# Kernel tuning notes

Hardware: AMD Instinct MI355X
Metric: run time of the kernel (lower is better)

Reference implementation:

```python
import jax, jax.numpy as jnp
import numpy as np

H = 8       # heads
DH = 64     # dim_head
EPS = 1e-5  # LayerNorm eps (torch default)


def _ln(x, g, b):
    m = x.mean(-1, keepdims=True)
    v = x.var(-1, keepdims=True)
    return (x - m) / jnp.sqrt(v + EPS) * g + b


def setup_inputs() -> dict:
    key = jax.random.key(0)
    ks = jax.random.split(key, 8)
    B, N, D = 2, 2048, 512
    s = lambda k, shape: jax.random.normal(k, shape, jnp.float32) * 0.02
    return {
        "q": jax.random.normal(ks[0], (B, N, D), jnp.float32),
        "k": jax.random.normal(ks[1], (B, N, D), jnp.float32),
        "v": jax.random.normal(ks[2], (B, N, D), jnp.float32),
        "ln_g": jnp.ones((D,), jnp.float32),
        "ln_b": jnp.zeros((D,), jnp.float32),
        "W_in": s(ks[3], (H * DH, D)),          # Linear(dim, inner_dim, bias=False)
        "wp_w1": s(ks[4], (DH, 2 * DH)),         # Linear(2*dim_head, dim_head)
        "wp_b1": jnp.zeros((DH,), jnp.float32),
        "wp_ln_g": jnp.ones((DH,), jnp.float32),
        "wp_ln_b": jnp.zeros((DH,), jnp.float32),
        "wp_w2": s(ks[5], (1, DH)),              # Linear(dim_head, 1)
        "wp_b2": jnp.zeros((1,), jnp.float32),
        "W_out": s(ks[6], (D, H * DH)),          # Linear(inner_dim, dim)
        "b_out": jnp.zeros((D,), jnp.float32),
    }


def reference(q, k, v, ln_g, ln_b, W_in, wp_w1, wp_b1, wp_ln_g, wp_ln_b,
              wp_w2, wp_b2, W_out, b_out):
    B, N, D = q.shape

    def proj(t):
        x = _ln(t, ln_g, ln_b) @ W_in.T                 # [B, N, H*DH]
        return x.reshape(B, N, H, DH).transpose(2, 0, 1, 3)  # [H, B, N, DH]

    fq, fk, fv = proj(q), proj(k), proj(v)

    # cosine similarity component
    dots = jnp.einsum('hbnd,hbmd->hbnm', fq, fk)        # [H, B, N, N]
    qn = jnp.linalg.norm(fq, axis=-1)                   # [H, B, N]
    kn = jnp.linalg.norm(fk, axis=-1)
    cosine = dots / (qn[..., :, None] * kn[..., None, :])

    # mean-centered covariance component
    qc = fq - fq.mean(-1, keepdims=True)
    kc = fk - fk.mean(-1, keepdims=True)
    cov = jnp.einsum('hbnd,hbmd->hbnm', qc, kc) / DH    # [H, B, N, N]

    # dynamic per-head blend weight
    qg = fq.mean((1, 2))                                # [H, DH]
    kg = fk.mean((1, 2))
    feat = jnp.concatenate([qg, kg], axis=-1)           # [H, 2*DH]
    hid = jax.nn.relu(_ln(feat @ wp_w1.T + wp_b1, wp_ln_g, wp_ln_b))
    w = jax.nn.sigmoid(hid @ wp_w2.T + wp_b2)           # [H, 1]
    w = w.reshape(H, 1, 1, 1)

    blend = (1.0 - w) * cosine + w * cov                # no softmax in cosine variant
    out = jnp.einsum('hbnm,hbmd->hbnd', blend, fv)      # [H, B, N, DH]
    out = out.transpose(1, 2, 0, 3).reshape(B, N, H * DH)
    return out @ W_out.T + b_out
```

## Files before the change

### kernel.cpp

```cpp
#include <hip/hip_runtime.h>
#include <stdint.h>

#define CH 8
#define CDH 64
#define CB 2
#define CN 2048
#define CD 512

typedef float f32x4 __attribute__((ext_vector_type(4)));
typedef __bf16 bf16x8 __attribute__((ext_vector_type(8)));
typedef unsigned short u16;
typedef unsigned int u32;

#define MFMA(a, b, c) __builtin_amdgcn_mfma_f32_16x16x32_bf16((a), (b), (c), 0, 0, 0)
#define GLOAD16(g, l)                                                              \
  __builtin_amdgcn_global_load_lds((const __attribute__((address_space(1))) void*)(g), \
                                   (__attribute__((address_space(3))) void*)(l), 16, 0, 0)

__device__ __forceinline__ u16 f2bf(float f) {
  union { float f; unsigned u; } c; c.f = f;
  return (u16)((c.u + 0x7FFFu + ((c.u >> 16) & 1u)) >> 16);
}
__device__ __forceinline__ float bf2f(u16 h) {
  union { unsigned u; float f; } c; c.u = ((unsigned)h) << 16;
  return c.f;
}

__global__ __launch_bounds__(256) void ln_convw_kernel(const float* __restrict__ q,
                                                       const float* __restrict__ k,
                                                       const float* __restrict__ v,
                                                       const float* __restrict__ g,
                                                       const float* __restrict__ bb,
                                                       u16* __restrict__ xln,
                                                       const float* __restrict__ wi_f,
                                                       const float* __restrict__ wo_f,
                                                       u16* __restrict__ wi,
                                                       u16* __restrict__ wo) {
  int row = blockIdx.x;
  int tid = threadIdx.x;
  if (row >= 12288) {
    int i = (row - 12288) * 256 + tid;
    wi[i] = f2bf(wi_f[i]);
    wo[i] = f2bf(wo_f[i]);
    return;
  }
  int t = row >> 12;
  int rr = row & 4095;
  const float* src = (t == 0 ? q : (t == 1 ? k : v)) + (size_t)rr * CD;
  float x0 = src[tid], x1 = src[tid + 256];
  float s = x0 + x1, s2 = x0 * x0 + x1 * x1;
#pragma unroll
  for (int m = 1; m < 64; m <<= 1) { s += __shfl_xor(s, m); s2 += __shfl_xor(s2, m); }
  __shared__ float red[8];
  int w = tid >> 6;
  if ((tid & 63) == 0) { red[w] = s; red[4 + w] = s2; }
  __syncthreads();
  s = red[0] + red[1] + red[2] + red[3];
  s2 = red[4] + red[5] + red[6] + red[7];
  float mean = s * (1.f / 512.f);
  float var = s2 * (1.f / 512.f) - mean * mean;
  float rstd = rsqrtf(var + 1e-5f);
  u16* dst = xln + (size_t)row * CD;
  dst[tid]       = f2bf((x0 - mean) * rstd * g[tid] + bb[tid]);
  dst[tid + 256] = f2bf((x1 - mean) * rstd * g[tid + 256] + bb[tid + 256]);
}

template <int OUT_BF16, int ADD_BIAS, int MODE>
__global__ __launch_bounds__(256) void gemm_bt(const u16* __restrict__ A,
                                               const u16* __restrict__ Bt,
                                               void* __restrict__ Cout,
                                               const float* __restrict__ bias,
                                               float* __restrict__ iqn,
                                               float* __restrict__ ikn,
                                               float* __restrict__ qgp,
                                               float* __restrict__ kgp,
                                               u16* __restrict__ fkT,
                                               u16* __restrict__ fvT) {
  __shared__ u16 S[4][8192];
#define AL_(s) (S[s])
#define BL_(s) (S[2 + (s)])
  int tm = blockIdx.x * 128, tn = blockIdx.y * 128;
  int tid = threadIdx.x;
  int w = tid >> 6, l = tid & 63;
  int wr = w >> 1, wc = w & 1;
  int lo = l & 15, hi = l >> 4;

  f32x4 zz = {0.f, 0.f, 0.f, 0.f};
  f32x4 acc[4][4];
#pragma unroll
  for (int mi = 0; mi < 4; mi++)
#pragma unroll
    for (int ni = 0; ni < 4; ni++) acc[mi][ni] = zz;

  int rowA = 8 * w + (l >> 3);
  int sl = l & 7;

#pragma unroll
  for (int i = 0; i < 4; i++) {
    int rl = rowA + 32 * i;
    int sp = sl ^ (rl & 7);
    GLOAD16(A + (size_t)(tm + rl) * CD + sp * 8, (char*)AL_(0) + w * 1024 + i * 4096);
    GLOAD16(Bt + (size_t)(tn + rl) * CD + sp * 8, (char*)BL_(0) + w * 1024 + i * 4096);
  }
  __syncthreads();

  int cur = 0;
  for (int kt = 0; kt < 8; ++kt) {
    if (kt + 1 < 8) {
      int nxt = cur ^ 1;
#pragma unroll
      for (int i = 0; i < 4; i++) {
        int rl = rowA + 32 * i;
        int sp = sl ^ (rl & 7);
        GLOAD16(A + (size_t)(tm + rl) * CD + (kt + 1) * 64 + sp * 8,
                (char*)AL_(nxt) + w * 1024 + i * 4096);
        GLOAD16(Bt + (size_t)(tn + rl) * CD + (kt + 1) * 64 + sp * 8,
                (char*)BL_(nxt) + w * 1024 + i * 4096);
      }
    }
    const u16* Ac = AL_(cur);
    const u16* Bc = BL_(cur);
#pragma unroll
    for (int kk = 0; kk < 2; kk++) {
      bf16x8 af[4], bfr[4];
#pragma unroll
      for (int mi = 0; mi < 4; mi++) {
        int row = wr * 64 + mi * 16 + lo;
        int slot = (hi + 4 * kk) ^ (row & 7);
        af[mi] = *(const bf16x8*)&Ac[row * 64 + slot * 8];
      }
#pragma unroll
      for (int ni = 0; ni < 4; ni++) {
        int row = wc * 64 + ni * 16 + lo;
        int slot = (hi + 4 * kk) ^ (row & 7);
        bfr[ni] = *(const bf16x8*)&Bc[row * 64 + slot * 8];
      }
#pragma unroll
      for (int mi = 0; mi < 4; mi++)
#pragma unroll
        for (int ni = 0; ni < 4; ni++)
          acc[mi][ni] = MFMA(af[mi], bfr[ni], acc[mi][ni]);
    }
    if (kt + 1 < 8) {
      __syncthreads();
      cur ^= 1;
    }
  }

  if (MODE == 1) {
    int tblk = blockIdx.x;
    int h = blockIdx.y * 2 + wc;
    if (tblk < 32) {
#pragma unroll
      for (int mi = 0; mi < 4; mi++)
#pragma unroll
        for (int rg = 0; rg < 4; rg++) {
          float s2 = 0.f;
#pragma unroll
          for (int ni = 0; ni < 4; ni++) {
            float vv = acc[mi][ni][rg];
            s2 += vv * vv;
          }
#pragma unroll
          for (int m = 1; m < 16; m <<= 1) s2 += __shfl_xor(s2, m);
          if (lo == 0) {
            int rloc = tm + wr * 64 + mi * 16 + hi * 4 + rg;
            int b = rloc >> 11, n = rloc & 2047;
            iqn[((size_t)h * 2 + b) * CN + n] = rsqrtf(s2);
          }
        }
      float cs[4];
#pragma unroll
      for (int ni = 0; ni < 4; ni++) {
        float s = 0.f;
#pragma unroll
        for (int mi = 0; mi < 4; mi++)
#pragma unroll
          for (int rg = 0; rg < 4; rg++) s += acc[mi][ni][rg];
        s += __shfl_xor(s, 16);
        s += __shfl_xor(s, 32);
        cs[ni] = s;
      }
      __syncthreads();
      float* redl = (float*)&S[0][0];
      if (hi == 0)
#pragma unroll
        for (int ni = 0; ni < 4; ni++) redl[((wr * 2 + wc) * 4 + ni) * 16 + lo] = cs[ni];
      __syncthreads();
      if (wr == 0 && hi == 0) {
#pragma unroll
        for (int ni = 0; ni < 4; ni++) {
          float vsum = redl[((0 * 2 + wc) * 4 + ni) * 16 + lo] +
                       redl[((1 * 2 + wc) * 4 + ni) * 16 + lo];
          qgp[(tblk * 8 + h) * 64 + ni * 16 + lo] = vsum;
        }
      }
    } else {
      bool isk = tblk < 64;
      u16* dstT = isk ? fkT : fvT;
      int rloc0 = tm - (isk ? 4096 : 8192);
      int bb2 = rloc0 >> 11, n0 = rloc0 & 2047;
      float csk[4];
      if (isk) {
#pragma unroll
        for (int mi = 0; mi < 4; mi++)
#pragma unroll
          for (int rg = 0; rg < 4; rg++) {
            float s2 = 0.f;
#pragma unroll
            for (int ni = 0; ni < 4; ni++) {
              float vv = acc[mi][ni][rg];
              s2 += vv * vv;
            }
#pragma unroll
            for (int m = 1; m < 16; m <<= 1) s2 += __shfl_xor(s2, m);
            if (lo == 0) {
              int n = n0 + wr * 64 + mi * 16 + hi * 4 + rg;
              ikn[((size_t)h * 2 + bb2) * CN + n] = rsqrtf(s2);
            }
          }
#pragma unroll
        for (int ni = 0; ni < 4; ni++) {
          float s = 0.f;
#pragma unroll
          for (int mi = 0; mi < 4; mi++)
#pragma unroll
            for (int rg = 0; rg < 4; rg++) s += acc[mi][ni][rg];
          s += __shfl_xor(s, 16);
          s += __shfl_xor(s, 32);
          csk[ni] = s;
        }
      }
      __syncthreads();
      u16* Sf = &S[0][0];
      int reg = wc * 2 + wr;
#pragma unroll
      for (int mi = 0; mi < 4; mi++)
#pragma unroll
        for (int ni = 0; ni < 4; ni++) {
          int d = ni * 16 + lo;
          int m0 = mi * 16 + hi * 4;
          u16 t4[4];
#pragma unroll
          for (int rg = 0; rg < 4; rg++) t4[rg] = f2bf(acc[mi][ni][rg]);
          int off = (reg * 64 + d) * 64 + (m0 ^ ((d & 7) << 3));
          *(uint2*)&Sf[off] = *(const uint2*)t4;
        }
      __syncthreads();
      {
        int head = tid >> 7, c = tid & 127;
        int hg = blockIdx.y * 2 + head;
        size_t base = ((size_t)(hg * 2 + bb2)) * 64 * CN;
#pragma unroll
        for (int p = 0; p < 8; p++) {
          int flat = p * 128 + c;
          int d = flat >> 4, mc = flat & 15;
          int wr2 = mc >> 3, m64 = (mc & 7) * 8;
          int off = ((head * 2 + wr2) * 64 + d) * 64 + (m64 ^ ((d & 7) << 3));
          bf16x8 vv = *(const bf16x8*)&Sf[off];
          *(bf16x8*)&dstT[base + (size_t)d * CN + n0 + mc * 8] = vv;
        }
      }
      if (isk) {
        __syncthreads();
        float* redl = (float*)&S[0][0];
        if (hi == 0)
#pragma unroll
          for (int ni = 0; ni < 4; ni++) redl[((wr * 2 + wc) * 4 + ni) * 16 + lo] = csk[ni];
        __syncthreads();
        if (wr == 0 && hi == 0) {
#pragma unroll
          for (int ni = 0; ni < 4; ni++) {
            float vsum = redl[((0 * 2 + wc) * 4 + ni) * 16 + lo] +
                         redl[((1 * 2 + wc) * 4 + ni) * 16 + lo];
            kgp[((tblk - 32) * 8 + h) * 64 + ni * 16 + lo] = vsum;
          }
        }
      }
      return;
    }
  }

#pragma unroll
  for (int mi = 0; mi < 4; mi++)
#pragma unroll
    for (int ni = 0; ni < 4; ni++) {
      int col = tn + wc * 64 + ni * 16 + lo;
      float bv = ADD_BIAS ? bias[col] : 0.f;
#pragma unroll
      for (int rg = 0; rg < 4; rg++) {
        int rowg = tm + wr * 64 + mi * 16 + hi * 4 + rg;
        float vout = acc[mi][ni][rg] + bv;
        if (OUT_BF16)
          ((u16*)Cout)[(size_t)rowg * CD + col] = f2bf(vout);
        else
          ((float*)Cout)[(size_t)rowg * CD + col] = vout;
      }
    }
#undef AL_
#undef BL_
}

__global__ __launch_bounds__(256) void gemm_M(const u16* __restrict__ fkT,
                                              const u16* __restrict__ fvT,
                                              const float* __restrict__ ikn,
                                              float* __restrict__ Mpart) {
  int bid = blockIdx.x;
  int hb = bid & 15, ms = bid >> 4;
  int tid = threadIdx.x, w = tid >> 6, l = tid & 63;
  int lo = l & 15, hi = l >> 4;

  __shared__ u16 GM[6][4096];
#define AK_(s) (GM[s])
#define AKH_(s) (GM[2 + (s)])
#define BV_(s) (GM[4 + (s)])

  const u16* Ab = fkT + (size_t)hb * 64 * CN;
  const u16* Vb = fvT + (size_t)hb * 64 * CN;
  const float* ikb = ikn + (size_t)hb * CN;

  f32x4 zz = {0.f, 0.f, 0.f, 0.f};
  f32x4 acc[2][4];
#pragma unroll
  for (int mat = 0; mat < 2; mat++)
#pragma unroll
    for (int dt = 0; dt < 4; dt++) acc[mat][dt] = zz;

  int rls = 8 * w + (l >> 3);
  int sls = l & 7;

  bf16x8 areg[2];
  f32x4 ikreg[2][2];

  auto STAGEGL = [&](int kt, int slot) {
    int mc = ms * 512 + kt * 64;
#pragma unroll
    for (int i = 0; i < 2; i++) {
      int row = rls + 32 * i;
      int sp = sls ^ (row & 7);
      GLOAD16(Ab + (size_t)row * CN + mc + sp * 8, (char*)AK_(slot) + w * 1024 + i * 4096);
      GLOAD16(Vb + (size_t)row * CN + mc + sp * 8, (char*)BV_(slot) + w * 1024 + i * 4096);
    }
  };
  auto LOADA = [&](int kt) {
    int mc = ms * 512 + kt * 64;
#pragma unroll
    for (int i = 0; i < 2; i++) {
      int row = rls + 32 * i;
      int sp = sls ^ (row & 7);
      areg[i] = *(const bf16x8*)&Ab[(size_t)row * CN + mc + sp * 8];
      ikreg[i][0] = *(const f32x4*)&ikb[mc + sp * 8];
      ikreg[i][1] = *(const f32x4*)&ikb[mc + sp * 8 + 4];
    }
  };
  auto WRITEA = [&](int slot) {
#pragma unroll
    for (int i = 0; i < 2; i++) {
      u16 outp[8];
#pragma unroll
      for (int j = 0; j < 4; j++) outp[j] = f2bf((float)areg[i][j] * ikreg[i][0][j]);
#pragma unroll
      for (int j = 0; j < 4; j++) outp[4 + j] = f2bf((float)areg[i][4 + j] * ikreg[i][1][j]);
      *(bf16x8*)((char*)AKH_(slot) + w * 1024 + i * 4096 + l * 16) = *(const bf16x8*)outp;
    }
  };

  LOADA(0);
  STAGEGL(0, 0);
  WRITEA(0);
  __syncthreads();

  int cur = 0;
  for (int kt = 0; kt < 8; ++kt) {
    if (kt + 1 < 8) {
      LOADA(kt + 1);
      STAGEGL(kt + 1, cur ^ 1);
    }
#pragma unroll
    for (int kk = 0; kk < 2; kk++) {
      int arow = w * 16 + lo;
      int aslot = (hi + 4 * kk) ^ (arow & 7);
      bf16x8 af = *(const bf16x8*)&AK_(cur)[arow * 64 + aslot * 8];
      bf16x8 afh = *(const bf16x8*)&AKH_(cur)[arow * 64 + aslot * 8];
#pragma unroll
      for (int dt = 0; dt < 4; dt++) {
        int brow = dt * 16 + lo;
        int bslot = (hi + 4 * kk) ^ (brow & 7);
        bf16x8 bv = *(const bf16x8*)&BV_(cur)[brow * 64 + bslot * 8];
        acc[0][dt] = MFMA(afh, bv, acc[0][dt]);
        acc[1][dt] = MFMA(af, bv, acc[1][dt]);
      }
    }
    if (kt + 1 < 8) {
      WRITEA(cur ^ 1);
      __syncthreads();
      cur ^= 1;
    }
  }

  float* outp = Mpart + ((size_t)(hb * 4 + ms)) * 8192;
#pragma unroll
  for (int mat = 0; mat < 2; mat++)
#pragma unroll
    for (int dt = 0; dt < 4; dt++) {
      int d = dt * 16 + lo;
#pragma unroll
      for (int rg = 0; rg < 4; rg++) {
        int j = mat * 64 + w * 16 + hi * 4 + rg;
        outp[j * 64 + d] = acc[mat][dt][rg];
      }
    }
#undef AK_
#undef AKH_
#undef BV_
}

__global__ __launch_bounds__(256) void reduceM_mlp(const float* __restrict__ Mpart,
                                                   const float* __restrict__ qgp,
                                                   const float* __restrict__ kgp,
                                                   const float* __restrict__ w1,
                                                   const float* __restrict__ b1,
                                                   const float* __restrict__ lng,
                                                   const float* __restrict__ lnb,
                                                   const float* __restrict__ w2,
                                                   const float* __restrict__ b2,
                                                   u16* __restrict__ Bmat) {
  int hb = blockIdx.x;
  int h = hb >> 1;
  int tid = threadIdx.x;
  __shared__ float qg[64], kg[64], abg[3];
  if (tid < 64) {
    float s1 = 0.f, s2 = 0.f;
#pragma unroll
    for (int c = 0; c < 32; c++) {
      s1 += qgp[(c * 8 + h) * 64 + tid];
      s2 += kgp[(c * 8 + h) * 64 + tid];
    }
    qg[tid] = s1 * (1.f / 4096.f);
    kg[tid] = s2 * (1.f / 4096.f);
  }
  __syncthreads();
  if (tid < 64) {
    float acc = b1[tid];
#pragma unroll 8
    for (int i = 0; i < 64; i++)
      acc += qg[i] * w1[tid * 128 + i] + kg[i] * w1[tid * 128 + 64 + i];
    float s1 = acc, s2 = acc * acc;
#pragma unroll
    for (int m = 1; m < 64; m <<= 1) { s1 += __shfl_xor(s1, m); s2 += __shfl_xor(s2, m); }
    float mean = s1 * (1.f / 64.f);
    float var = s2 * (1.f / 64.f) - mean * mean;
    float y = (acc - mean) * rsqrtf(var + 1e-5f) * lng[tid] + lnb[tid];
    float hid = fmaxf(y, 0.f);
    float t = hid * w2[tid];
#pragma unroll
    for (int m = 1; m < 64; m <<= 1) t += __shfl_xor(t, m);
    float wv = 1.f / (1.f + expf(-(t + b2[0])));
    if (tid == 0) { abg[0] = 1.f - wv; abg[1] = wv * (1.f / 64.f); abg[2] = wv; }
  }
  __syncthreads();
  float alpha = abg[0], beta = abg[1], gamma = abg[2];

  __shared__ float Ms[128 * 65];
  __shared__ float S2s[64];
#pragma unroll
  for (int e = 0; e < 32; e++) {
    int idx = e * 256 + tid;
    int j = idx >> 6, d = idx & 63;
    float s = 0.f;
#pragma unroll
    for (int ms = 0; ms < 4; ms++)
      s += Mpart[((size_t)(hb * 4 + ms)) * 8192 + idx];
    Ms[j * 65 + d] = s;
  }
  __syncthreads();
  if (tid < 64) {
    float s = 0.f;
#pragma unroll
    for (int i = 0; i < 64; i++) s += Ms[(64 + i) * 65 + tid];
    S2s[tid] = s;
  }
  __syncthreads();
#pragma unroll
  for (int e = 0; e < 32; e++) {
    int idx = e * 256 + tid;
    int jr = idx >> 6, ic = idx & 63;
    float v;
    if (jr < 64) v = alpha * Ms[ic * 65 + jr];
    else {
      int d = jr - 64;
      v = beta * Ms[(64 + ic) * 65 + d] - (gamma * (1.f / 4096.f)) * S2s[d];
    }
    Bmat[(size_t)hb * 8192 + idx] = f2bf(v);
  }
}

__global__ __launch_bounds__(256) void gemm_out(const u16* __restrict__ F0,
                                                const u16* __restrict__ Bmat,
                                                const float* __restrict__ iqn,
                                                u16* __restrict__ A2) {
  int bid = blockIdx.x;
  int hb = bid >> 4, qt = bid & 15;
  int b = hb & 1, h = hb >> 1;
  int tid = threadIdx.x, w = tid >> 6, l = tid & 63;
  int lo = l & 15, hi = l >> 4;
  int qbase = qt * 128;

  const u16* Bm = Bmat + (size_t)hb * 8192;
  bf16x8 bm[8][2];
#pragma unroll
  for (int jt = 0; jt < 8; jt++)
#pragma unroll
    for (int kk = 0; kk < 2; kk++)
      bm[jt][kk] = *(const bf16x8*)&Bm[(jt * 16 + lo) * 64 + hi * 8 + kk * 32];

  f32x4 zz = {0.f, 0.f, 0.f, 0.f};
  f32x4 acc[2][8];
#pragma unroll
  for (int f = 0; f < 2; f++)
#pragma unroll
    for (int jt = 0; jt < 8; jt++) acc[f][jt] = zz;

#pragma unroll
  for (int f = 0; f < 2; f++) {
    const u16* qp = F0 + ((size_t)(b * CN + qbase + w * 32 + f * 16 + lo)) * CD +
                    h * 64 + hi * 8;
    bf16x8 a0 = *(const bf16x8*)qp;
    bf16x8 a1 = *(const bf16x8*)(qp + 32);
#pragma unroll
    for (int jt = 0; jt < 8; jt++) {
      acc[f][jt] = MFMA(a0, bm[jt][0], acc[f][jt]);
      acc[f][jt] = MFMA(a1, bm[jt][1], acc[f][jt]);
    }
  }

  const float* iqn_hb = iqn + (size_t)hb * CN;
#pragma unroll
  for (int f = 0; f < 2; f++) {
    float iqv[4];
    int nb = qbase + w * 32 + f * 16 + hi * 4;
#pragma unroll
    for (int rg = 0; rg < 4; rg++) iqv[rg] = iqn_hb[nb + rg];
#pragma unroll
    for (int jt = 0; jt < 4; jt++) {
      int d = jt * 16 + lo;
#pragma unroll
      for (int rg = 0; rg < 4; rg++) {
        float vout = iqv[rg] * acc[f][jt][rg] + acc[f][jt + 4][rg];
        int n = nb + rg;
        A2[((size_t)(b * CN + n)) * CD + h * 64 + d] = f2bf(vout);
      }
    }
  }
}

extern "C" void kernel_launch(void* const* d_in, const int* in_sizes, int n_in,
                              void* d_out, int out_size, void* d_ws, size_t ws_size,
                              hipStream_t stream) {
  const float* q = (const float*)d_in[0];
  const float* k = (const float*)d_in[1];
  const float* v = (const float*)d_in[2];
  const float* ln_g = (const float*)d_in[3];
  const float* ln_b = (const float*)d_in[4];
  const float* W_in = (const float*)d_in[5];
  const float* wp_w1 = (const float*)d_in[6];
  const float* wp_b1 = (const float*)d_in[7];
  const float* wp_lng = (const float*)d_in[8];
  const float* wp_lnb = (const float*)d_in[9];
  const float* wp_w2 = (const float*)d_in[10];
  const float* wp_b2 = (const float*)d_in[11];
  const float* W_out = (const float*)d_in[12];
  const float* b_out = (const float*)d_in[13];

  char* ws = (char*)d_ws;
  u16* xln = (u16*)(ws + 0);
  u16* F0 = (u16*)(ws + 12582912);
  u16* Wi = (u16*)(ws + 16777216);
  u16* Wo = (u16*)(ws + 17301504);
  u16* fkT = (u16*)(ws + 17825792);
  u16* fvT = (u16*)(ws + 22020096);
  u16* A2 = (u16*)(ws + 26214400);
  float* iqn = (float*)(ws + 30408704);
  float* ikn = (float*)(ws + 30539776);
  float* qgp = (float*)(ws + 30670848);
  float* kgp = (float*)(ws + 30736384);
  float* Mpart = (float*)(ws + 30801920);
  u16* Bmat = (u16*)(ws + 32899072);

  ln_convw_kernel<<<13312, 256, 0, stream>>>(q, k, v, ln_g, ln_b, xln,
                                             W_in, W_out, Wi, Wo);
  gemm_bt<1, 0, 1><<<dim3(96, 4), 256, 0, stream>>>(xln, Wi, (void*)F0, nullptr,
                                                    iqn, ikn, qgp, kgp, fkT, fvT);
  gemm_M<<<64, 256, 0, stream>>>(fkT, fvT, ikn, Mpart);
  reduceM_mlp<<<16, 256, 0, stream>>>(Mpart, qgp, kgp, wp_w1, wp_b1,
                                      wp_lng, wp_lnb, wp_w2, wp_b2, Bmat);
  gemm_out<<<256, 256, 0, stream>>>(F0, Bmat, iqn, A2);
  gemm_bt<0, 1, 0><<<dim3(32, 4), 256, 0, stream>>>(A2, Wo, d_out, b_out,
                                                    nullptr, nullptr, nullptr,
                                                    nullptr, nullptr, nullptr);
}
```

Measured before the change: 61.54 us.

## Fold per-head blend matrices into output projection and merge launches

The per-head KV matrices are folded into the output projection weights, giving a per-batch 1024-wide combined weight. The final GEMM then reads a concatenated [normalized q | raw q] activation, which removes the separate gemm_out pass, the A2 intermediate and the iqn buffer. The M reduction and the blend-weight MLP are merged into one 16-block kernel that runs the full 2048-long reduction without split partials, cutting two launches. The trade-off is a lower-parallelism M kernel (16 blocks instead of 64), a doubled K in the final GEMM, and a larger F0 write.

```diff
diff --git a/kernel.cpp b/kernel.cpp
--- a/kernel.cpp
+++ b/kernel.cpp
@@ -10,7 +10,6 @@
 typedef float f32x4 __attribute__((ext_vector_type(4)));
 typedef __bf16 bf16x8 __attribute__((ext_vector_type(8)));
 typedef unsigned short u16;
-typedef unsigned int u32;
 
 #define MFMA(a, b, c) __builtin_amdgcn_mfma_f32_16x16x32_bf16((a), (b), (c), 0, 0, 0)
 #define GLOAD16(g, l)                                                              \
@@ -65,17 +64,14 @@
   dst[tid + 256] = f2bf((x1 - mean) * rstd * g[tid + 256] + bb[tid + 256]);
 }
 
-template <int OUT_BF16, int ADD_BIAS, int MODE>
-__global__ __launch_bounds__(256) void gemm_bt(const u16* __restrict__ A,
-                                               const u16* __restrict__ Bt,
-                                               void* __restrict__ Cout,
-                                               const float* __restrict__ bias,
-                                               float* __restrict__ iqn,
-                                               float* __restrict__ ikn,
-                                               float* __restrict__ qgp,
-                                               float* __restrict__ kgp,
-                                               u16* __restrict__ fkT,
-                                               u16* __restrict__ fvT) {
+__global__ __launch_bounds__(256) void gemm1(const u16* __restrict__ A,
+                                             const u16* __restrict__ Bt,
+                                             u16* __restrict__ F0cat,
+                                             float* __restrict__ ikn,
+                                             float* __restrict__ qgp,
+                                             float* __restrict__ kgp,
+                                             u16* __restrict__ fkT,
+                                             u16* __restrict__ fvT) {
   __shared__ u16 S[4][8192];
 #define AL_(s) (S[s])
 #define BL_(s) (S[2 + (s)])
@@ -147,10 +143,70 @@
     }
   }
 
-  if (MODE == 1) {
-    int tblk = blockIdx.x;
-    int h = blockIdx.y * 2 + wc;
-    if (tblk < 32) {
+  int tblk = blockIdx.x;
+  int h = blockIdx.y * 2 + wc;
+  if (tblk < 32) {
+    float rsq[4][4];
+#pragma unroll
+    for (int mi = 0; mi < 4; mi++)
+#pragma unroll
+      for (int rg = 0; rg < 4; rg++) {
+        float s2 = 0.f;
+#pragma unroll
+        for (int ni = 0; ni < 4; ni++) {
+          float vv = acc[mi][ni][rg];
+          s2 += vv * vv;
+        }
+#pragma unroll
+        for (int m = 1; m < 16; m <<= 1) s2 += __shfl_xor(s2, m);
+        rsq[mi][rg] = rsqrtf(s2);
+      }
+    float cs[4];
+#pragma unroll
+    for (int ni = 0; ni < 4; ni++) {
+      float s = 0.f;
+#pragma unroll
+      for (int mi = 0; mi < 4; mi++)
+#pragma unroll
+        for (int rg = 0; rg < 4; rg++) s += acc[mi][ni][rg];
+      s += __shfl_xor(s, 16);
+      s += __shfl_xor(s, 32);
+      cs[ni] = s;
+    }
+    __syncthreads();
+    float* redl = (float*)&S[0][0];
+    if (hi == 0)
+#pragma unroll
+      for (int ni = 0; ni < 4; ni++) redl[((wr * 2 + wc) * 4 + ni) * 16 + lo] = cs[ni];
+    __syncthreads();
+    if (wr == 0 && hi == 0) {
+#pragma unroll
+      for (int ni = 0; ni < 4; ni++) {
+        float vsum = redl[((0 * 2 + wc) * 4 + ni) * 16 + lo] +
+                     redl[((1 * 2 + wc) * 4 + ni) * 16 + lo];
+        qgp[(tblk * 8 + h) * 64 + ni * 16 + lo] = vsum;
+      }
+    }
+#pragma unroll
+    for (int mi = 0; mi < 4; mi++)
+#pragma unroll
+      for (int ni = 0; ni < 4; ni++) {
+        int gcol = tn + wc * 64 + ni * 16 + lo;
+#pragma unroll
+        for (int rg = 0; rg < 4; rg++) {
+          int rowg = tm + wr * 64 + mi * 16 + hi * 4 + rg;
+          float vv = acc[mi][ni][rg];
+          F0cat[(size_t)rowg * 1024 + gcol] = f2bf(rsq[mi][rg] * vv);
+          F0cat[(size_t)rowg * 1024 + 512 + gcol] = f2bf(vv);
+        }
+      }
+  } else {
+    bool isk = tblk < 64;
+    u16* dstT = isk ? fkT : fvT;
+    int rloc0 = tm - (isk ? 4096 : 8192);
+    int bb2 = rloc0 >> 11, n0 = rloc0 & 2047;
+    float csk[4];
+    if (isk) {
 #pragma unroll
       for (int mi = 0; mi < 4; mi++)
 #pragma unroll
@@ -164,12 +220,10 @@
 #pragma unroll
           for (int m = 1; m < 16; m <<= 1) s2 += __shfl_xor(s2, m);
           if (lo == 0) {
-            int rloc = tm + wr * 64 + mi * 16 + hi * 4 + rg;
-            int b = rloc >> 11, n = rloc & 2047;
-            iqn[((size_t)h * 2 + b) * CN + n] = rsqrtf(s2);
+            int n = n0 + wr * 64 + mi * 16 + hi * 4 + rg;
+            ikn[((size_t)h * 2 + bb2) * CN + n] = rsqrtf(s2);
           }
         }
-      float cs[4];
 #pragma unroll
       for (int ni = 0; ni < 4; ni++) {
         float s = 0.f;
@@ -179,134 +233,70 @@
           for (int rg = 0; rg < 4; rg++) s += acc[mi][ni][rg];
         s += __shfl_xor(s, 16);
         s += __shfl_xor(s, 32);
-        cs[ni] = s;
-      }
+        csk[ni] = s;
+      }
+    }
+    __syncthreads();
+    u16* Sf = &S[0][0];
+    int reg = wc * 2 + wr;
+#pragma unroll
+    for (int mi = 0; mi < 4; mi++)
+#pragma unroll
+      for (int ni = 0; ni < 4; ni++) {
+        int d = ni * 16 + lo;
+        int m0 = mi * 16 + hi * 4;
+        u16 t4[4];
+#pragma unroll
+        for (int rg = 0; rg < 4; rg++) t4[rg] = f2bf(acc[mi][ni][rg]);
+        int off = (reg * 64 + d) * 64 + (m0 ^ ((d & 7) << 3));
+        *(uint2*)&Sf[off] = *(const uint2*)t4;
+      }
+    __syncthreads();
+    {
+      int head = tid >> 7, c = tid & 127;
+      int hg = blockIdx.y * 2 + head;
+      size_t base = ((size_t)(hg * 2 + bb2)) * 64 * CN;
+#pragma unroll
+      for (int p = 0; p < 8; p++) {
+        int flat = p * 128 + c;
+        int d = flat >> 4, mc = flat & 15;
+        int wr2 = mc >> 3, m64 = (mc & 7) * 8;
+        int off = ((head * 2 + wr2) * 64 + d) * 64 + (m64 ^ ((d & 7) << 3));
+        bf16x8 vv = *(const bf16x8*)&Sf[off];
+        *(bf16x8*)&dstT[base + (size_t)d * CN + n0 + mc * 8] = vv;
+      }
+    }
+    if (isk) {
       __syncthreads();
       float* redl = (float*)&S[0][0];
       if (hi == 0)
 #pragma unroll
-        for (int ni = 0; ni < 4; ni++) redl[((wr * 2 + wc) * 4 + ni) * 16 + lo] = cs[ni];
+        for (int ni = 0; ni < 4; ni++) redl[((wr * 2 + wc) * 4 + ni) * 16 + lo] = csk[ni];
       __syncthreads();
       if (wr == 0 && hi == 0) {
 #pragma unroll
         for (int ni = 0; ni < 4; ni++) {
           float vsum = redl[((0 * 2 + wc) * 4 + ni) * 16 + lo] +
                        redl[((1 * 2 + wc) * 4 + ni) * 16 + lo];
-          qgp[(tblk * 8 + h) * 64 + ni * 16 + lo] = vsum;
+          kgp[((tblk - 32) * 8 + h) * 64 + ni * 16 + lo] = vsum;
         }
       }
-    } else {
-      bool isk = tblk < 64;
-      u16* dstT = isk ? fkT : fvT;
-      int rloc0 = tm - (isk ? 4096 : 8192);
-      int bb2 = rloc0 >> 11, n0 = rloc0 & 2047;
-      float csk[4];
-      if (isk) {
-#pragma unroll
-        for (int mi = 0; mi < 4; mi++)
-#pragma unroll
-          for (int rg = 0; rg < 4; rg++) {
-            float s2 = 0.f;
-#pragma unroll
-            for (int ni = 0; ni < 4; ni++) {
-              float vv = acc[mi][ni][rg];
-              s2 += vv * vv;
-            }
-#pragma unroll
-            for (int m = 1; m < 16; m <<= 1) s2 += __shfl_xor(s2, m);
-            if (lo == 0) {
-              int n = n0 + wr * 64 + mi * 16 + hi * 4 + rg;
-              ikn[((size_t)h * 2 + bb2) * CN + n] = rsqrtf(s2);
-            }
-          }
-#pragma unroll
-        for (int ni = 0; ni < 4; ni++) {
-          float s = 0.f;
-#pragma unroll
-          for (int mi = 0; mi < 4; mi++)
-#pragma unroll
-            for (int rg = 0; rg < 4; rg++) s += acc[mi][ni][rg];
-          s += __shfl_xor(s, 16);
-          s += __shfl_xor(s, 32);
-          csk[ni] = s;
-        }
-      }
-      __syncthreads();
-      u16* Sf = &S[0][0];
-      int reg = wc * 2 + wr;
-#pragma unroll
-      for (int mi = 0; mi < 4; mi++)
-#pragma unroll
-        for (int ni = 0; ni < 4; ni++) {
-          int d = ni * 16 + lo;
-          int m0 = mi * 16 + hi * 4;
-          u16 t4[4];
-#pragma unroll
-          for (int rg = 0; rg < 4; rg++) t4[rg] = f2bf(acc[mi][ni][rg]);
-          int off = (reg * 64 + d) * 64 + (m0 ^ ((d & 7) << 3));
-          *(uint2*)&Sf[off] = *(const uint2*)t4;
-        }
-      __syncthreads();
-      {
-        int head = tid >> 7, c = tid & 127;
-        int hg = blockIdx.y * 2 + head;
-        size_t base = ((size_t)(hg * 2 + bb2)) * 64 * CN;
-#pragma unroll
-        for (int p = 0; p < 8; p++) {
-          int flat = p * 128 + c;
-          int d = flat >> 4, mc = flat & 15;
-          int wr2 = mc >> 3, m64 = (mc & 7) * 8;
-          int off = ((head * 2 + wr2) * 64 + d) * 64 + (m64 ^ ((d & 7) << 3));
-          bf16x8 vv = *(const bf16x8*)&Sf[off];
-          *(bf16x8*)&dstT[base + (size_t)d * CN + n0 + mc * 8] = vv;
-        }
-      }
-      if (isk) {
-        __syncthreads();
-        float* redl = (float*)&S[0][0];
-        if (hi == 0)
-#pragma unroll
-          for (int ni = 0; ni < 4; ni++) redl[((wr * 2 + wc) * 4 + ni) * 16 + lo] = csk[ni];
-        __syncthreads();
-        if (wr == 0 && hi == 0) {
-#pragma unroll
-          for (int ni = 0; ni < 4; ni++) {
-            float vsum = redl[((0 * 2 + wc) * 4 + ni) * 16 + lo] +
-                         redl[((1 * 2 + wc) * 4 + ni) * 16 + lo];
-            kgp[((tblk - 32) * 8 + h) * 64 + ni * 16 + lo] = vsum;
-          }
-        }
-      }
-      return;
-    }
-  }
-
-#pragma unroll
-  for (int mi = 0; mi < 4; mi++)
-#pragma unroll
-    for (int ni = 0; ni < 4; ni++) {
-      int col = tn + wc * 64 + ni * 16 + lo;
-      float bv = ADD_BIAS ? bias[col] : 0.f;
-#pragma unroll
-      for (int rg = 0; rg < 4; rg++) {
-        int rowg = tm + wr * 64 + mi * 16 + hi * 4 + rg;
-        float vout = acc[mi][ni][rg] + bv;
-        if (OUT_BF16)
-          ((u16*)Cout)[(size_t)rowg * CD + col] = f2bf(vout);
-        else
-          ((float*)Cout)[(size_t)rowg * CD + col] = vout;
-      }
-    }
+    }
+  }
 #undef AL_
 #undef BL_
 }
 
-__global__ __launch_bounds__(256) void gemm_M(const u16* __restrict__ fkT,
-                                              const u16* __restrict__ fvT,
-                                              const float* __restrict__ ikn,
-                                              float* __restrict__ Mpart) {
-  int bid = blockIdx.x;
-  int hb = bid & 15, ms = bid >> 4;
+__global__ __launch_bounds__(256) void gemm_M_mlp_w(
+    const u16* __restrict__ fkT, const u16* __restrict__ fvT,
+    const float* __restrict__ ikn, const float* __restrict__ qgp,
+    const float* __restrict__ kgp, const float* __restrict__ w1,
+    const float* __restrict__ b1, const float* __restrict__ lng,
+    const float* __restrict__ lnb, const float* __restrict__ w2,
+    const float* __restrict__ b2, const u16* __restrict__ Wo,
+    u16* __restrict__ Wbig) {
+  int hb = blockIdx.x;
+  int h = hb >> 1, b = hb & 1;
   int tid = threadIdx.x, w = tid >> 6, l = tid & 63;
   int lo = l & 15, hi = l >> 4;
 
@@ -314,6 +304,38 @@
 #define AK_(s) (GM[s])
 #define AKH_(s) (GM[2 + (s)])
 #define BV_(s) (GM[4 + (s)])
+  __shared__ float abg[3];
+  __shared__ float Msf[64][65];
+  __shared__ float S2s[64];
+  __shared__ u16 M1b[64 * 72];
+  __shared__ u16 Cb[64 * 72];
+
+  if (tid < 64) {
+    float s1 = 0.f, s2 = 0.f;
+#pragma unroll
+    for (int c = 0; c < 32; c++) {
+      s1 += qgp[(c * 8 + h) * 64 + tid];
+      s2 += kgp[(c * 8 + h) * 64 + tid];
+    }
+    Msf[0][tid] = s1 * (1.f / 4096.f);
+    Msf[1][tid] = s2 * (1.f / 4096.f);
+    float acc = b1[tid];
+#pragma unroll 8
+    for (int i = 0; i < 64; i++)
+      acc += Msf[0][i] * w1[tid * 128 + i] + Msf[1][i] * w1[tid * 128 + 64 + i];
+    float t1 = acc, t2 = acc * acc;
+#pragma unroll
+    for (int m = 1; m < 64; m <<= 1) { t1 += __shfl_xor(t1, m); t2 += __shfl_xor(t2, m); }
+    float mean = t1 * (1.f / 64.f);
+    float var = t2 * (1.f / 64.f) - mean * mean;
+    float y = (acc - mean) * rsqrtf(var + 1e-5f) * lng[tid] + lnb[tid];
+    float hid = fmaxf(y, 0.f);
+    float t = hid * w2[tid];
+#pragma unroll
+    for (int m = 1; m < 64; m <<= 1) t += __shfl_xor(t, m);
+    float wv = 1.f / (1.f + expf(-(t + b2[0])));
+    if (tid == 0) { abg[0] = 1.f - wv; abg[1] = wv * (1.f / 64.f); abg[2] = wv; }
+  }
 
   const u16* Ab = fkT + (size_t)hb * 64 * CN;
   const u16* Vb = fvT + (size_t)hb * 64 * CN;
@@ -328,12 +350,11 @@
 
   int rls = 8 * w + (l >> 3);
   int sls = l & 7;
-
   bf16x8 areg[2];
   f32x4 ikreg[2][2];
 
   auto STAGEGL = [&](int kt, int slot) {
-    int mc = ms * 512 + kt * 64;
+    int mc = kt * 64;
 #pragma unroll
     for (int i = 0; i < 2; i++) {
       int row = rls + 32 * i;
@@ -343,7 +364,7 @@
     }
   };
   auto LOADA = [&](int kt) {
-    int mc = ms * 512 + kt * 64;
+    int mc = kt * 64;
 #pragma unroll
     for (int i = 0; i < 2; i++) {
       int row = rls + 32 * i;
@@ -371,8 +392,8 @@
   __syncthreads();
 
   int cur = 0;
-  for (int kt = 0; kt < 8; ++kt) {
-    if (kt + 1 < 8) {
+  for (int kt = 0; kt < 32; ++kt) {
+    if (kt + 1 < 32) {
       LOADA(kt + 1);
       STAGEGL(kt + 1, cur ^ 1);
     }
@@ -391,167 +412,160 @@
         acc[1][dt] = MFMA(af, bv, acc[1][dt]);
       }
     }
-    if (kt + 1 < 8) {
+    if (kt + 1 < 32) {
       WRITEA(cur ^ 1);
       __syncthreads();
       cur ^= 1;
     }
   }
 
-  float* outp = Mpart + ((size_t)(hb * 4 + ms)) * 8192;
-#pragma unroll
-  for (int mat = 0; mat < 2; mat++)
-#pragma unroll
-    for (int dt = 0; dt < 4; dt++) {
-      int d = dt * 16 + lo;
+  __syncthreads();
+#pragma unroll
+  for (int dt = 0; dt < 4; dt++)
+#pragma unroll
+    for (int rg = 0; rg < 4; rg++)
+      Msf[w * 16 + hi * 4 + rg][dt * 16 + lo] = acc[1][dt][rg];
+  __syncthreads();
+  if (tid < 64) {
+    float s = 0.f;
+#pragma unroll
+    for (int i = 0; i < 64; i++) s += Msf[i][tid];
+    S2s[tid] = s;
+  }
+  __syncthreads();
+
+  float alpha = abg[0], beta = abg[1], g4 = abg[2] * (1.f / 4096.f);
+#pragma unroll
+  for (int dt = 0; dt < 4; dt++)
+#pragma unroll
+    for (int rg = 0; rg < 4; rg++) {
+      int i = w * 16 + hi * 4 + rg, d = dt * 16 + lo;
+      M1b[i * 72 + d] = f2bf(alpha * acc[0][dt][rg]);
+      Cb[i * 72 + d] = f2bf(beta * acc[1][dt][rg] - g4 * S2s[d]);
+    }
+  __syncthreads();
+
+  u16* Wb = Wbig + (size_t)b * 512 * 1024;
+#pragma unroll
+  for (int rf = 0; rf < 8; rf++) {
+    int dbase = w * 128 + rf * 16;
+    bf16x8 af[2];
+#pragma unroll
+    for (int kk = 0; kk < 2; kk++)
+      af[kk] = *(const bf16x8*)&Wo[(size_t)(dbase + lo) * 512 + h * 64 + kk * 32 + hi * 8];
+    f32x4 a1[4], a2[4];
+#pragma unroll
+    for (int cf = 0; cf < 4; cf++) { a1[cf] = zz; a2[cf] = zz; }
+#pragma unroll
+    for (int kk = 0; kk < 2; kk++)
+#pragma unroll
+      for (int cf = 0; cf < 4; cf++) {
+        bf16x8 m1 = *(const bf16x8*)&M1b[(cf * 16 + lo) * 72 + kk * 32 + hi * 8];
+        bf16x8 cb = *(const bf16x8*)&Cb[(cf * 16 + lo) * 72 + kk * 32 + hi * 8];
+        a1[cf] = MFMA(af[kk], m1, a1[cf]);
+        a2[cf] = MFMA(af[kk], cb, a2[cf]);
+      }
+#pragma unroll
+    for (int cf = 0; cf < 4; cf++)
 #pragma unroll
       for (int rg = 0; rg < 4; rg++) {
-        int j = mat * 64 + w * 16 + hi * 4 + rg;
-        outp[j * 64 + d] = acc[mat][dt][rg];
-      }
-    }
+        int dout = dbase + hi * 4 + rg;
+        int icol = cf * 16 + lo;
+        Wb[(size_t)dout * 1024 + h * 64 + icol] = f2bf(a1[cf][rg]);
+        Wb[(size_t)dout * 1024 + 512 + h * 64 + icol] = f2bf(a2[cf][rg]);
+      }
+  }
 #undef AK_
 #undef AKH_
 #undef BV_
 }
 
-__global__ __launch_bounds__(256) void reduceM_mlp(const float* __restrict__ Mpart,
-                                                   const float* __restrict__ qgp,
-                                                   const float* __restrict__ kgp,
-                                                   const float* __restrict__ w1,
-                                                   const float* __restrict__ b1,
-                                                   const float* __restrict__ lng,
-                                                   const float* __restrict__ lnb,
-                                                   const float* __restrict__ w2,
-                                                   const float* __restrict__ b2,
-                                                   u16* __restrict__ Bmat) {
-  int hb = blockIdx.x;
-  int h = hb >> 1;
+__global__ __launch_bounds__(256) void gemm_final(const u16* __restrict__ A,
+                                                  const u16* __restrict__ Wbig,
+                                                  const float* __restrict__ bias,
+                                                  float* __restrict__ Cout) {
+  __shared__ u16 Al[2][128 * 64];
+  __shared__ u16 Bl[2][128 * 64];
+  int tm = blockIdx.x * 128, tn = blockIdx.y * 128;
+  const u16* Bt = Wbig + (size_t)(tm >> 11) * 512 * 1024;
   int tid = threadIdx.x;
-  __shared__ float qg[64], kg[64], abg[3];
-  if (tid < 64) {
-    float s1 = 0.f, s2 = 0.f;
-#pragma unroll
-    for (int c = 0; c < 32; c++) {
-      s1 += qgp[(c * 8 + h) * 64 + tid];
-      s2 += kgp[(c * 8 + h) * 64 + tid];
-    }
-    qg[tid] = s1 * (1.f / 4096.f);
-    kg[tid] = s2 * (1.f / 4096.f);
-  }
-  __syncthreads();
-  if (tid < 64) {
-    float acc = b1[tid];
-#pragma unroll 8
-    for (int i = 0; i < 64; i++)
-      acc += qg[i] * w1[tid * 128 + i] + kg[i] * w1[tid * 128 + 64 + i];
-    float s1 = acc, s2 = acc * acc;
-#pragma unroll
-    for (int m = 1; m < 64; m <<= 1) { s1 += __shfl_xor(s1, m); s2 += __shfl_xor(s2, m); }
-    float mean = s1 * (1.f / 64.f);
-    float var = s2 * (1.f / 64.f) - mean * mean;
-    float y = (acc - mean) * rsqrtf(var + 1e-5f) * lng[tid] + lnb[tid];
-    float hid = fmaxf(y, 0.f);
-    float t = hid * w2[tid];
-#pragma unroll
-    for (int m = 1; m < 64; m <<= 1) t += __shfl_xor(t, m);
-    float wv = 1.f / (1.f + expf(-(t + b2[0])));
-    if (tid == 0) { abg[0] = 1.f - wv; abg[1] = wv * (1.f / 64.f); abg[2] = wv; }
-  }
-  __syncthreads();
-  float alpha = abg[0], beta = abg[1], gamma = abg[2];
-
-  __shared__ float Ms[128 * 65];
-  __shared__ float S2s[64];
-#pragma unroll
-  for (int e = 0; e < 32; e++) {
-    int idx = e * 256 + tid;
-    int j = idx >> 6, d = idx & 63;
-    float s = 0.f;
-#pragma unroll
-    for (int ms = 0; ms < 4; ms++)
-      s += Mpart[((size_t)(hb * 4 + ms)) * 8192 + idx];
-    Ms[j * 65 + d] = s;
-  }
-  __syncthreads();
-  if (tid < 64) {
-    float s = 0.f;
-#pragma unroll
-    for (int i = 0; i < 64; i++) s += Ms[(64 + i) * 65 + tid];
-    S2s[tid] = s;
-  }
-  __syncthreads();
-#pragma unroll
-  for (int e = 0; e < 32; e++) {
-    int idx = e * 256 + tid;
-    int jr = idx >> 6, ic = idx & 63;
-    float v;
-    if (jr < 64) v = alpha * Ms[ic * 65 + jr];
-    else {
-      int d = jr - 64;
-      v = beta * Ms[(64 + ic) * 65 + d] - (gamma * (1.f / 4096.f)) * S2s[d];
-    }
-    Bmat[(size_t)hb * 8192 + idx] = f2bf(v);
-  }
-}
-
-__global__ __launch_bounds__(256) void gemm_out(const u16* __restrict__ F0,
-                                                const u16* __restrict__ Bmat,
-                                                const float* __restrict__ iqn,
-                                                u16* __restrict__ A2) {
-  int bid = blockIdx.x;
-  int hb = bid >> 4, qt = bid & 15;
-  int b = hb & 1, h = hb >> 1;
-  int tid = threadIdx.x, w = tid >> 6, l = tid & 63;
+  int w = tid >> 6, l = tid & 63;
+  int wr = w >> 1, wc = w & 1;
   int lo = l & 15, hi = l >> 4;
-  int qbase = qt * 128;
-
-  const u16* Bm = Bmat + (size_t)hb * 8192;
-  bf16x8 bm[8][2];
-#pragma unroll
-  for (int jt = 0; jt < 8; jt++)
-#pragma unroll
-    for (int kk = 0; kk < 2; kk++)
-      bm[jt][kk] = *(const bf16x8*)&Bm[(jt * 16 + lo) * 64 + hi * 8 + kk * 32];
 
   f32x4 zz = {0.f, 0.f, 0.f, 0.f};
-  f32x4 acc[2][8];
-#pragma unroll
-  for (int f = 0; f < 2; f++)
-#pragma unroll
-    for (int jt = 0; jt < 8; jt++) acc[f][jt] = zz;
-
-#pragma unroll
-  for (int f = 0; f < 2; f++) {
-    const u16* qp = F0 + ((size_t)(b * CN + qbase + w * 32 + f * 16 + lo)) * CD +
-                    h * 64 + hi * 8;
-    bf16x8 a0 = *(const bf16x8*)qp;
-    bf16x8 a1 = *(const bf16x8*)(qp + 32);
-#pragma unroll
-    for (int jt = 0; jt < 8; jt++) {
-      acc[f][jt] = MFMA(a0, bm[jt][0], acc[f][jt]);
-      acc[f][jt] = MFMA(a1, bm[jt][1], acc[f][jt]);
-    }
-  }
-
-  const float* iqn_hb = iqn + (size_t)hb * CN;
-#pragma unroll
-  for (int f = 0; f < 2; f++) {
-    float iqv[4];
-    int nb = qbase + w * 32 + f * 16 + hi * 4;
-#pragma unroll
-    for (int rg = 0; rg < 4; rg++) iqv[rg] = iqn_hb[nb + rg];
-#pragma unroll
-    for (int jt = 0; jt < 4; jt++) {
-      int d = jt * 16 + lo;
+  f32x4 acc[4][4];
+#pragma unroll
+  for (int mi = 0; mi < 4; mi++)
+#pragma unroll
+    for (int ni = 0; ni < 4; ni++) acc[mi][ni] = zz;
+
+  int rowA = 8 * w + (l >> 3);
+  int sl = l & 7;
+
+#pragma unroll
+  for (int i = 0; i < 4; i++) {
+    int rl = rowA + 32 * i;
+    int sp = sl ^ (rl & 7);
+    GLOAD16(A + (size_t)(tm + rl) * 1024 + sp * 8, (char*)Al[0] + w * 1024 + i * 4096);
+    GLOAD16(Bt + (size_t)(tn + rl) * 1024 + sp * 8, (char*)Bl[0] + w * 1024 + i * 4096);
+  }
+  __syncthreads();
+
+  int cur = 0;
+  for (int kt = 0; kt < 16; ++kt) {
+    if (kt + 1 < 16) {
+      int nxt = cur ^ 1;
+#pragma unroll
+      for (int i = 0; i < 4; i++) {
+        int rl = rowA + 32 * i;
+        int sp = sl ^ (rl & 7);
+        GLOAD16(A + (size_t)(tm + rl) * 1024 + (kt + 1) * 64 + sp * 8,
+                (char*)Al[nxt] + w * 1024 + i * 4096);
+        GLOAD16(Bt + (size_t)(tn + rl) * 1024 + (kt + 1) * 64 + sp * 8,
+                (char*)Bl[nxt] + w * 1024 + i * 4096);
+      }
+    }
+    const u16* Ac = Al[cur];
+    const u16* Bc = Bl[cur];
+#pragma unroll
+    for (int kk = 0; kk < 2; kk++) {
+      bf16x8 af[4], bfr[4];
+#pragma unroll
+      for (int mi = 0; mi < 4; mi++) {
+        int row = wr * 64 + mi * 16 + lo;
+        int slot = (hi + 4 * kk) ^ (row & 7);
+        af[mi] = *(const bf16x8*)&Ac[row * 64 + slot * 8];
+      }
+#pragma unroll
+      for (int ni = 0; ni < 4; ni++) {
+        int row = wc * 64 + ni * 16 + lo;
+        int slot = (hi + 4 * kk) ^ (row & 7);
+        bfr[ni] = *(const bf16x8*)&Bc[row * 64 + slot * 8];
+      }
+#pragma unroll
+      for (int mi = 0; mi < 4; mi++)
+#pragma unroll
+        for (int ni = 0; ni < 4; ni++)
+          acc[mi][ni] = MFMA(af[mi], bfr[ni], acc[mi][ni]);
+    }
+    if (kt + 1 < 16) {
+      __syncthreads();
+      cur ^= 1;
+    }
+  }
+#pragma unroll
+  for (int mi = 0; mi < 4; mi++)
+#pragma unroll
+    for (int ni = 0; ni < 4; ni++) {
+      int col = tn + wc * 64 + ni * 16 + lo;
+      float bv = bias[col];
 #pragma unroll
       for (int rg = 0; rg < 4; rg++) {
-        float vout = iqv[rg] * acc[f][jt][rg] + acc[f][jt + 4][rg];
-        int n = nb + rg;
-        A2[((size_t)(b * CN + n)) * CD + h * 64 + d] = f2bf(vout);
-      }
-    }
-  }
+        int rowg = tm + wr * 64 + mi * 16 + hi * 4 + rg;
+        Cout[(size_t)rowg * CD + col] = acc[mi][ni][rg] + bv;
+      }
+    }
 }
 
 extern "C" void kernel_launch(void* const* d_in, const int* in_sizes, int n_in,
@@ -574,28 +588,20 @@
 
   char* ws = (char*)d_ws;
   u16* xln = (u16*)(ws + 0);
-  u16* F0 = (u16*)(ws + 12582912);
-  u16* Wi = (u16*)(ws + 16777216);
-  u16* Wo = (u16*)(ws + 17301504);
-  u16* fkT = (u16*)(ws + 17825792);
-  u16* fvT = (u16*)(ws + 22020096);
-  u16* A2 = (u16*)(ws + 26214400);
-  float* iqn = (float*)(ws + 30408704);
-  float* ikn = (float*)(ws + 30539776);
-  float* qgp = (float*)(ws + 30670848);
-  float* kgp = (float*)(ws + 30736384);
-  float* Mpart = (float*)(ws + 30801920);
-  u16* Bmat = (u16*)(ws + 32899072);
+  u16* F0cat = (u16*)(ws + 12582912);
+  u16* Wi = (u16*)(ws + 20971520);
+  u16* Wo = (u16*)(ws + 21495808);
+  u16* fkT = (u16*)(ws + 22020096);
+  u16* fvT = (u16*)(ws + 26214400);
+  float* ikn = (float*)(ws + 30408704);
+  float* qgp = (float*)(ws + 30539776);
+  float* kgp = (float*)(ws + 30605312);
+  u16* Wbig = (u16*)(ws + 30670848);
 
   ln_convw_kernel<<<13312, 256, 0, stream>>>(q, k, v, ln_g, ln_b, xln,
                                              W_in, W_out, Wi, Wo);
-  gemm_bt<1, 0, 1><<<dim3(96, 4), 256, 0, stream>>>(xln, Wi, (void*)F0, nullptr,
-                                                    iqn, ikn, qgp, kgp, fkT, fvT);
-  gemm_M<<<64, 256, 0, stream>>>(fkT, fvT, ikn, Mpart);
-  reduceM_mlp<<<16, 256, 0, stream>>>(Mpart, qgp, kgp, wp_w1, wp_b1,
-                                      wp_lng, wp_lnb, wp_w2, wp_b2, Bmat);
-  gemm_out<<<256, 256, 0, stream>>>(F0, Bmat, iqn, A2);
-  gemm_bt<0, 1, 0><<<dim3(32, 4), 256, 0, stream>>>(A2, Wo, d_out, b_out,
-                                                    nullptr, nullptr, nullptr,
-                                                    nullptr, nullptr, nullptr);
+  gemm1<<<dim3(96, 4), 256, 0, stream>>>(xln, Wi, F0cat, ikn, qgp, kgp, fkT, fvT);
+  gemm_M_mlp_w<<<16, 256, 0, stream>>>(fkT, fvT, ikn, qgp, kgp, wp_w1, wp_b1,
+                                       wp_lng, wp_lnb, wp_w2, wp_b2, Wo, Wbig);
+  gemm_final<<<dim3(32, 4), 256, 0, stream>>>(F0cat, Wbig, b_out, (float*)d_out);
 }
```

Measured after the change: 98.40 us. +59.9%, slower.
